# Kernel tuning notes

Measured on AMD Instinct MI355X. Metric: run time of the kernel, lower is better.

Reference implementation:

```python
import jax, jax.numpy as jnp
import numpy as np

B, S, D, H = 2, 2048, 1024, 16
HD = D // H  # head_dim = 64


def setup_inputs() -> dict:
    key = jax.random.key(0)
    ks = jax.random.split(key, 6)
    scale_h = 1.0 / np.sqrt(HD)
    scale_d = 1.0 / np.sqrt(D)
    return {
        "x": jax.random.normal(ks[0], (B, S, D), dtype=jnp.float32),
        # per-head projection weights (CausalAttention Linear(head_dim, head_dim, bias=False)), stacked over heads
        "Wq": jax.random.normal(ks[1], (H, HD, HD), dtype=jnp.float32) * scale_h,
        "Wk": jax.random.normal(ks[2], (H, HD, HD), dtype=jnp.float32) * scale_h,
        "Wv": jax.random.normal(ks[3], (H, HD, HD), dtype=jnp.float32) * scale_h,
        # final nn.Linear(dim, dim): y = x @ Wo + bo (Wo stored already transposed vs torch)
        "Wo": jax.random.normal(ks[4], (D, D), dtype=jnp.float32) * scale_d,
        "bo": jax.random.normal(ks[5], (D,), dtype=jnp.float32) * 0.01,
    }


def reference(x, Wq, Wk, Wv, Wo, bo):
    b, s, d = x.shape
    h, hd, _ = Wq.shape
    # head h sees contiguous channel slice x[:, :, h*hd:(h+1)*hd]
    xh = x.reshape(b, s, h, hd)                                  # [B,S,H,HD]
    q = jnp.einsum("bshd,hde->bhse", xh, Wq)                     # [B,H,S,HD]
    k = jnp.einsum("bshd,hde->bhse", xh, Wk)
    v = jnp.einsum("bshd,hde->bhse", xh, Wv)
    scores = jnp.einsum("bhse,bhte->bhst", q, k) * (hd ** -0.5)  # [B,H,S,S]
    causal = jnp.tril(jnp.ones((s, s), dtype=bool))
    scores = jnp.where(causal, scores, jnp.finfo(scores.dtype).min)
    attn = jax.nn.softmax(scores, axis=-1)
    out = jnp.einsum("bhst,bhtd->bshd", attn, v)                 # [B,S,H,HD]
    # torch.stack(out_list, dim=-1) -> [B,S,HD,H]; reshape -> interleaved channels
    out = jnp.swapaxes(out, -1, -2).reshape(b, s, d)
    return out @ Wo + bo
```

## Files before the change

kernel.cpp:

```cpp
#include <hip/hip_runtime.h>

typedef __attribute__((ext_vector_type(8))) _Float16 half8;
typedef __attribute__((ext_vector_type(2))) __fp16 fp16x2;
typedef __attribute__((ext_vector_type(4))) float f32x4;
typedef __attribute__((ext_vector_type(16))) float f32x16;

constexpr int Bc = 2, Sc = 2048, Dc = 1024, Hc = 16, HDc = 64;

#define PKU(a, b) __builtin_bit_cast(unsigned, __builtin_amdgcn_cvt_pkrtz((a), (b)))

#define PACK_STORE(vA0, vA1, vA2, vA3, vB0, vB1, vB2, vB3, ptr) {        \
  unsigned W0 = PKU(vA0, vA1), W1 = PKU(vA2, vA3);                       \
  unsigned X0 = PKU(vB0, vB1), X1 = PKU(vB2, vB3);                       \
  unsigned s0_ = (unsigned)__shfl_xor((int)(hi ? W0 : X0), 32);          \
  unsigned s1_ = (unsigned)__shfl_xor((int)(hi ? W1 : X1), 32);          \
  union { unsigned u[4]; half8 h8; } P_;                                 \
  P_.u[0] = hi ? s0_ : W0; P_.u[1] = hi ? s1_ : W1;                      \
  P_.u[2] = hi ? X0 : s0_; P_.u[3] = hi ? X1 : s1_;                      \
  *(half8*)(ptr) = P_.h8; }

__global__ __launch_bounds__(256) void prep_w(const float* __restrict__ Wq,
                                              const float* __restrict__ Wk,
                                              const float* __restrict__ Wv,
                                              _Float16* __restrict__ WT) {
  const int m = blockIdx.x >> 4;
  const int h = blockIdx.x & 15;
  const float* src = (m == 0 ? Wq : (m == 1 ? Wk : Wv)) + (size_t)h * 4096;
  const float scale = (m == 0) ? 0.125f * 1.44269504088896f : 1.0f;
  __shared__ float T[64][65];
  const int tid = threadIdx.x;
#pragma unroll
  for (int i = 0; i < 4; ++i) {
    int r = (tid >> 4) + 16 * i, c4 = (tid & 15) * 4;
    *(float4*)&T[r][c4] = *(const float4*)(src + r * 64 + c4);
  }
  __syncthreads();
  _Float16* dst = WT + ((size_t)m * 16 + h) * 4096;
#pragma unroll
  for (int i = 0; i < 4; ++i) {
    int e = (tid >> 4) + 16 * i, d4 = (tid & 15) * 4;
    union { _Float16 hh[4]; unsigned long long u; } pk;
#pragma unroll
    for (int j = 0; j < 4; ++j) pk.hh[j] = (_Float16)(T[d4 + j][e] * scale);
    *(unsigned long long*)(dst + (size_t)e * 64 + d4) = pk.u;
  }
}

__global__ __launch_bounds__(256) void prep_wo(const float* __restrict__ Wo,
                                               _Float16* __restrict__ WoT) {
  __shared__ float T[64][68];
  const int hh = blockIdx.x;
  const int n0 = blockIdx.y * 64;
  const int tid = threadIdx.x;
#pragma unroll
  for (int i = 0; i < 4; ++i) {
    int g = tid + i * 256;
    int e = g >> 4, c4 = (g & 15) * 4;
    *(float4*)&T[e][c4] = *(const float4*)(Wo + (size_t)(e * 16 + hh) * Dc + n0 + c4);
  }
  __syncthreads();
#pragma unroll
  for (int i = 0; i < 4; ++i) {
    int g = tid + i * 256;
    int c = g >> 4, e4 = (g & 15) * 4;
    union { _Float16 h[4]; unsigned long long u; } pk;
    pk.h[0] = (_Float16)T[e4 + 0][c];
    pk.h[1] = (_Float16)T[e4 + 1][c];
    pk.h[2] = (_Float16)T[e4 + 2][c];
    pk.h[3] = (_Float16)T[e4 + 3][c];
    *(unsigned long long*)(WoT + (size_t)(n0 + c) * Dc + hh * 64 + e4) = pk.u;
  }
}

__global__ __launch_bounds__(256) void qkv_proj(
    const float* __restrict__ x, const _Float16* __restrict__ WT,
    _Float16* __restrict__ Qp, _Float16* __restrict__ Kp,
    _Float16* __restrict__ Vp) {
  const int h = blockIdx.x & 15;
  const int st = (blockIdx.x >> 4) & 15;
  const int b = blockIdx.x >> 8;
  const int s0 = st * 128;
  const int tid = threadIdx.x;
  const int l = tid & 63, w = tid >> 6;
  const int lq = l & 31, hi = l >> 5;

  half8 xa[4];
  const float* xrow = x + ((size_t)(b * Sc + s0 + 32 * w + lq)) * Dc + h * 64 + hi * 8;
#pragma unroll
  for (int c = 0; c < 4; ++c) {
    float4 u0 = *(const float4*)(xrow + c * 16);
    float4 u1 = *(const float4*)(xrow + c * 16 + 4);
    union { fp16x2 h2[4]; half8 h8; } pk;
    pk.h2[0] = __builtin_amdgcn_cvt_pkrtz(u0.x, u0.y);
    pk.h2[1] = __builtin_amdgcn_cvt_pkrtz(u0.z, u0.w);
    pk.h2[2] = __builtin_amdgcn_cvt_pkrtz(u1.x, u1.y);
    pk.h2[3] = __builtin_amdgcn_cvt_pkrtz(u1.z, u1.w);
    xa[c] = pk.h8;
  }

  const _Float16* WTq = WT + (size_t)h * 4096;
  const _Float16* WTk = WT + (size_t)(16 + h) * 4096;
  const _Float16* WTv = WT + (size_t)(32 + h) * 4096;
  f32x16 Qt[2] = {}, Kt[2] = {}, Vd[2] = {};
#pragma unroll
  for (int et = 0; et < 2; ++et) {
#pragma unroll
    for (int c = 0; c < 4; ++c) {
      const int off = (32 * et + lq) * 64 + c * 16 + hi * 8;
      half8 wqf = *(const half8*)(WTq + off);
      half8 wkf = *(const half8*)(WTk + off);
      half8 wvf = *(const half8*)(WTv + off);
      Qt[et] = __builtin_amdgcn_mfma_f32_32x32x16_f16(wqf, xa[c], Qt[et], 0, 0, 0);
      Kt[et] = __builtin_amdgcn_mfma_f32_32x32x16_f16(wkf, xa[c], Kt[et], 0, 0, 0);
      Vd[et] = __builtin_amdgcn_mfma_f32_32x32x16_f16(xa[c], wvf, Vd[et], 0, 0, 0);
    }
  }
  const int bh = b * Hc + h;
  const int qt_ = 4 * st + w;
  const int ktile = 2 * st + (w >> 1);
  _Float16* qdst = Qp + (((size_t)(bh * 64 + qt_) * 4) << 9) + (l << 3);
  _Float16* kdst = Kp + (((size_t)((bh * 32 + ktile) * 8) + (w & 1) * 4) << 9) + (l << 3);
  _Float16* vdst = Vp + (((size_t)(bh * 32 + ktile) * 8) << 9) + (l << 3);

  PACK_STORE(Qt[0][0], Qt[0][1], Qt[0][2], Qt[0][3], Qt[0][4], Qt[0][5], Qt[0][6], Qt[0][7], qdst + (0 << 9));
  PACK_STORE(Qt[0][8], Qt[0][9], Qt[0][10], Qt[0][11], Qt[0][12], Qt[0][13], Qt[0][14], Qt[0][15], qdst + (1 << 9));
  PACK_STORE(Qt[1][0], Qt[1][1], Qt[1][2], Qt[1][3], Qt[1][4], Qt[1][5], Qt[1][6], Qt[1][7], qdst + (2 << 9));
  PACK_STORE(Qt[1][8], Qt[1][9], Qt[1][10], Qt[1][11], Qt[1][12], Qt[1][13], Qt[1][14], Qt[1][15], qdst + (3 << 9));

  PACK_STORE(Kt[0][0], Kt[0][1], Kt[0][2], Kt[0][3], Kt[0][4], Kt[0][5], Kt[0][6], Kt[0][7], kdst + (0 << 9));
  PACK_STORE(Kt[0][8], Kt[0][9], Kt[0][10], Kt[0][11], Kt[0][12], Kt[0][13], Kt[0][14], Kt[0][15], kdst + (1 << 9));
  PACK_STORE(Kt[1][0], Kt[1][1], Kt[1][2], Kt[1][3], Kt[1][4], Kt[1][5], Kt[1][6], Kt[1][7], kdst + (2 << 9));
  PACK_STORE(Kt[1][8], Kt[1][9], Kt[1][10], Kt[1][11], Kt[1][12], Kt[1][13], Kt[1][14], Kt[1][15], kdst + (3 << 9));

#pragma unroll
  for (int et = 0; et < 2; ++et) {
    PACK_STORE(Vd[et][0], Vd[et][1], Vd[et][2], Vd[et][3], Vd[et][4], Vd[et][5], Vd[et][6], Vd[et][7],
               vdst + ((size_t)(et * 4 + ((2 * w + 0) & 3)) << 9));
    PACK_STORE(Vd[et][8], Vd[et][9], Vd[et][10], Vd[et][11], Vd[et][12], Vd[et][13], Vd[et][14], Vd[et][15],
               vdst + ((size_t)(et * 4 + ((2 * w + 1) & 3)) << 9));
  }
}

#define DOB(t, q0v) (((t) * 64 + 32) <= (q0v) + 31)

#define LOADQ(qtv) {                                                          \
  const _Float16* qb_ = Qp + (((size_t)(bh * 64 + (qtv)) * 4) << 9) + (l << 3); \
  _Pragma("unroll") for (int c = 0; c < 4; ++c)                               \
    qf[c] = *(const half8*)(qb_ + (c << 9)); }

#define STEP(t, q0v) {                                                        \
  const int k0 = (t) * 64;                                                    \
  const bool doB = DOB(t, q0v);                                               \
  const int q_g = (q0v) + lq;                                                 \
  const _Float16* kp8 = Kp + (((kvb + (t)) * 8) << 9) + (l << 3);             \
  const _Float16* vp8 = Vp + (((kvb + (t)) * 8) << 9) + (l << 3);             \
  f32x16 SA = {}, SB = {};                                                    \
  {                                                                           \
    half8 ka[4], kb[4];                                                       \
    _Pragma("unroll") for (int c = 0; c < 4; ++c)                             \
      ka[c] = *(const half8*)(kp8 + (c << 9));                                \
    if (doB) {                                                                \
      _Pragma("unroll") for (int c = 0; c < 4; ++c)                           \
        kb[c] = *(const half8*)(kp8 + ((4 + c) << 9));                        \
    }                                                                         \
    __builtin_amdgcn_s_setprio(1);                                            \
    _Pragma("unroll") for (int c = 0; c < 4; ++c)                             \
      SA = __builtin_amdgcn_mfma_f32_32x32x16_f16(ka[c], qf[c], SA, 0, 0, 0); \
    if (doB) {                                                                \
      _Pragma("unroll") for (int c = 0; c < 4; ++c)                           \
        SB = __builtin_amdgcn_mfma_f32_32x32x16_f16(kb[c], qf[c], SB, 0, 0, 0); \
    }                                                                         \
    __builtin_amdgcn_s_setprio(0);                                            \
  }                                                                           \
  if (k0 + 63 > (q0v)) {                                                      \
    _Pragma("unroll") for (int r = 0; r < 16; ++r) {                          \
      const int kk = k0 + (r & 3) + 8 * (r >> 2) + 4 * hi;                    \
      if (kk > q_g) SA[r] = -1e30f;                                           \
      if (doB && kk + 32 > q_g) SB[r] = -1e30f;                               \
    }                                                                         \
  }                                                                           \
  float mx = -1e30f;                                                          \
  _Pragma("unroll") for (int r = 0; r < 16; ++r) mx = fmaxf(mx, SA[r]);       \
  if (doB) {                                                                  \
    _Pragma("unroll") for (int r = 0; r < 16; ++r) mx = fmaxf(mx, SB[r]);     \
  }                                                                           \
  mx = fmaxf(mx, __shfl_xor(mx, 32));                                         \
  if (!__all(mx <= m_run + 4.0f)) {                                           \
    const float mnew = fmaxf(m_run, mx);                                      \
    const float corr = __builtin_amdgcn_exp2f(m_run - mnew);                  \
    l_run *= corr;                                                            \
    _Pragma("unroll") for (int r = 0; r < 16; ++r) { OA[r] *= corr; OB[r] *= corr; } \
    m_run = mnew;                                                             \
  }                                                                           \
  float ls = 0.f;                                                             \
  _Pragma("unroll") for (int ch = 0; ch < 4; ++ch) {                          \
    if (ch < (doB ? 4 : 2)) {                                                 \
      half8 va = *(const half8*)(vp8 + (ch << 9));                            \
      half8 vb = *(const half8*)(vp8 + ((4 + ch) << 9));                      \
      float p0, p1, p2, p3, p4, p5, p6, p7;                                   \
      if (ch < 2) {                                                           \
        const int base = ch * 8;                                              \
        p0 = __builtin_amdgcn_exp2f(SA[base + 0] - m_run);                    \
        p1 = __builtin_amdgcn_exp2f(SA[base + 1] - m_run);                    \
        p2 = __builtin_amdgcn_exp2f(SA[base + 2] - m_run);                    \
        p3 = __builtin_amdgcn_exp2f(SA[base + 3] - m_run);                    \
        p4 = __builtin_amdgcn_exp2f(SA[base + 4] - m_run);                    \
        p5 = __builtin_amdgcn_exp2f(SA[base + 5] - m_run);                    \
        p6 = __builtin_amdgcn_exp2f(SA[base + 6] - m_run);                    \
        p7 = __builtin_amdgcn_exp2f(SA[base + 7] - m_run);                    \
      } else {                                                                \
        const int base = (ch - 2) * 8;                                        \
        p0 = __builtin_amdgcn_exp2f(SB[base + 0] - m_run);                    \
        p1 = __builtin_amdgcn_exp2f(SB[base + 1] - m_run);                    \
        p2 = __builtin_amdgcn_exp2f(SB[base + 2] - m_run);                    \
        p3 = __builtin_amdgcn_exp2f(SB[base + 3] - m_run);                    \
        p4 = __builtin_amdgcn_exp2f(SB[base + 4] - m_run);                    \
        p5 = __builtin_amdgcn_exp2f(SB[base + 5] - m_run);                    \
        p6 = __builtin_amdgcn_exp2f(SB[base + 6] - m_run);                    \
        p7 = __builtin_amdgcn_exp2f(SB[base + 7] - m_run);                    \
      }                                                                       \
      ls += ((p0 + p1) + (p2 + p3)) + ((p4 + p5) + (p6 + p7));                \
      unsigned W0 = PKU(p0, p1), W1 = PKU(p2, p3);                            \
      unsigned W2 = PKU(p4, p5), W3 = PKU(p6, p7);                            \
      unsigned sw0 = (unsigned)__shfl_xor((int)(hi ? W0 : W2), 32);           \
      unsigned sw1 = (unsigned)__shfl_xor((int)(hi ? W1 : W3), 32);           \
      union { unsigned u[4]; half8 h; } pa;                                   \
      pa.u[0] = hi ? sw0 : W0;                                                \
      pa.u[1] = hi ? sw1 : W1;                                                \
      pa.u[2] = hi ? W2 : sw0;                                                \
      pa.u[3] = hi ? W3 : sw1;                                                \
      __builtin_amdgcn_s_setprio(1);                                          \
      OA = __builtin_amdgcn_mfma_f32_32x32x16_f16(va, pa.h, OA, 0, 0, 0);     \
      OB = __builtin_amdgcn_mfma_f32_32x32x16_f16(vb, pa.h, OB, 0, 0, 0);     \
      __builtin_amdgcn_s_setprio(0);                                          \
    }                                                                         \
  }                                                                           \
  ls += __shfl_xor(ls, 32);                                                   \
  l_run += ls; }

#define RUN_RANGE(t0, t1, q0v) {                                              \
  for (int t = (t0); t < (t1); ++t) { STEP(t, q0v); } }

#define PUBLISH(slot) {                                                       \
  _Pragma("unroll") for (int r = 0; r < 16; ++r) {                            \
    Osh[slot][l][r] = OA[r]; Osh[slot][l][16 + r] = OB[r];                    \
  }                                                                           \
  mls[slot][0][l] = m_run; mls[slot][1][l] = l_run; }

#define RESET() {                                                             \
  _Pragma("unroll") for (int r = 0; r < 16; ++r) { OA[r] = 0.f; OB[r] = 0.f; } \
  m_run = -1e30f; l_run = 0.f; }

#define MERGE(slot) {                                                         \
  const float ms = mls[slot][0][l], lsv = mls[slot][1][l];                    \
  const float mm = fmaxf(m_run, ms);                                          \
  const float c0 = __builtin_amdgcn_exp2f(m_run - mm);                        \
  const float c1 = __builtin_amdgcn_exp2f(ms - mm);                           \
  _Pragma("unroll") for (int r = 0; r < 16; ++r) {                            \
    OA[r] = OA[r] * c0 + Osh[slot][l][r] * c1;                                \
    OB[r] = OB[r] * c0 + Osh[slot][l][16 + r] * c1;                           \
  }                                                                           \
  l_run = l_run * c0 + lsv * c1; m_run = mm; }

#define STORE_OUT(q0v) {                                                      \
  const float inv = 1.f / l_run;                                              \
  _Float16* op = attC + ((size_t)b * Sc + (q0v) + lq) * Dc + h * 64;          \
  _Pragma("unroll") for (int g = 0; g < 4; ++g) {                             \
    union { _Float16 hh[4]; unsigned long long u; } pA, pB;                   \
    _Pragma("unroll") for (int jj = 0; jj < 4; ++jj) {                        \
      pA.hh[jj] = (_Float16)(OA[4 * g + jj] * inv);                           \
      pB.hh[jj] = (_Float16)(OB[4 * g + jj] * inv);                           \
    }                                                                         \
    *(unsigned long long*)(op + 8 * g + 4 * hi) = pA.u;                       \
    *(unsigned long long*)(op + 32 + 8 * g + 4 * hi) = pB.u;                  \
  } }

__global__ __launch_bounds__(256, 3) void flash_attn(
    const _Float16* __restrict__ Qp, const _Float16* __restrict__ Kp,
    const _Float16* __restrict__ Vp, _Float16* __restrict__ attC) {
  const int i = blockIdx.x;
  const int bh = (i & 7) * 4 + ((i >> 3) & 3);
  const int p = i >> 5;
  const int qlong = 63 - p, qshort = p;
  const int NTL = qlong / 2 + 1;
  const int NTS = qshort / 2 + 1;
  const int q0L = qlong * 32, q0S = qshort * 32;
  const int b = bh >> 4, h = bh & 15;
  const int tid = threadIdx.x;
  const int wv = tid >> 6, l = tid & 63;
  const int lq = l & 31, hi = l >> 5;
  const size_t kvb = (size_t)bh * 32;

  __shared__ float Osh[3][64][33];
  __shared__ float mls[3][2][64];

  half8 qf[4];
  f32x16 OA = {}, OB = {};
  float m_run = -1e30f, l_run = 0.f;

  if (wv == 0) {
    LOADQ(qlong);
    RUN_RANGE(0, 8, q0L);
  } else if (wv == 1) {
    LOADQ(qlong);
    RUN_RANGE(8, 16, q0L);
    PUBLISH(0);
  } else if (wv == 2) {
    LOADQ(qlong);
    const int e2 = NTL < 24 ? NTL : 24;
    RUN_RANGE(16, e2, q0L);
    PUBLISH(1);
    RESET();
    if (24 - NTL > 0) {
      LOADQ(qshort);
      RUN_RANGE(0, 24 - NTL, q0S);
    }
  } else {
    if (NTL > 24) {
      LOADQ(qlong);
      RUN_RANGE(24, NTL, q0L);
      PUBLISH(2);
      RESET();
      LOADQ(qshort);
      RUN_RANGE(0, NTS, q0S);
      STORE_OUT(q0S);
    } else {
      LOADQ(qshort);
      RUN_RANGE(24 - NTL, NTS, q0S);
      PUBLISH(2);
    }
  }
  __syncthreads();
  if (wv == 0) {
    MERGE(0);
    MERGE(1);
    if (NTL > 24) { MERGE(2); }
    STORE_OUT(q0L);
  } else if (wv == 2 && NTL <= 24) {
    MERGE(2);
    STORE_OUT(q0S);
  }
}

__global__ __launch_bounds__(256) void out_proj(
    const _Float16* __restrict__ attC, const _Float16* __restrict__ WoT,
    const float* __restrict__ bo, float* __restrict__ out) {
  const int m0 = blockIdx.x * 64, n0 = blockIdx.y * 64;
  __shared__ __align__(16) _Float16 Alds[64][40];
  __shared__ __align__(16) _Float16 Blds[64][40];
  const int tid = threadIdx.x;
  const int l = tid & 63, w = tid >> 6;
  const int lr = l & 15, lg = l >> 4;
  f32x4 acc[4] = {};
  for (int kt = 0; kt < 32; ++kt) {
    const int k0 = kt * 32;
    {
      const int r = tid >> 2, c8 = (tid & 3) * 8;
      *(half8*)&Alds[r][c8] = *(const half8*)(attC + (size_t)(m0 + r) * Dc + k0 + c8);
      *(half8*)&Blds[r][c8] = *(const half8*)(WoT + (size_t)(n0 + r) * Dc + k0 + c8);
    }
    __syncthreads();
    half8 bf = *(const half8*)&Blds[w * 16 + lr][lg * 8];
#pragma unroll
    for (int i2 = 0; i2 < 4; ++i2) {
      half8 af = *(const half8*)&Alds[i2 * 16 + lr][lg * 8];
      acc[i2] = __builtin_amdgcn_mfma_f32_16x16x32_f16(af, bf, acc[i2], 0, 0, 0);
    }
    __syncthreads();
  }
  const int n = n0 + w * 16 + lr;
  const float bias = bo[n];
#pragma unroll
  for (int i2 = 0; i2 < 4; ++i2)
#pragma unroll
    for (int r = 0; r < 4; ++r) {
      const int m = m0 + i2 * 16 + lg * 4 + r;
      out[(size_t)m * Dc + n] = acc[i2][r] + bias;
    }
}

extern "C" void kernel_launch(void* const* d_in, const int* in_sizes, int n_in,
                              void* d_out, int out_size, void* d_ws, size_t ws_size,
                              hipStream_t stream) {
  const float* x  = (const float*)d_in[0];
  const float* Wq = (const float*)d_in[1];
  const float* Wk = (const float*)d_in[2];
  const float* Wv = (const float*)d_in[3];
  const float* Wo = (const float*)d_in[4];
  const float* bo = (const float*)d_in[5];
  float* out = (float*)d_out;
  char* ws = (char*)d_ws;
  _Float16* Qp   = (_Float16*)(ws);
  _Float16* Kp   = (_Float16*)(ws + (size_t)(8  << 20));
  _Float16* Vp   = (_Float16*)(ws + (size_t)(16 << 20));
  _Float16* WoT  = (_Float16*)(ws + (size_t)(24 << 20));
  _Float16* WT   = (_Float16*)(ws + (size_t)(26 << 20));
  _Float16* attC = (_Float16*)(ws + (size_t)(26 << 20));

  prep_w<<<dim3(48), dim3(256), 0, stream>>>(Wq, Wk, Wv, WT);
  prep_wo<<<dim3(16, 16), dim3(256), 0, stream>>>(Wo, WoT);
  qkv_proj<<<dim3(512), dim3(256), 0, stream>>>(x, WT, Qp, Kp, Vp);
  flash_attn<<<dim3(1024), dim3(256), 0, stream>>>(Qp, Kp, Vp, attC);
  out_proj<<<dim3(64, 16), dim3(256), 0, stream>>>(attC, WoT, bo, out);
}
```

Before: 86.91 us.

## Stage x via swizzled LDS, hoist V loads, widen out_proj N tile

Three independent changes. qkv_proj now loads x coalesced into a swizzled shared-memory tile before building its MFMA fragments, replacing strided per-lane global reads. flash_attn issues all V fragment loads early, before masking and softmax, so their latency overlaps that work; this costs more registers. out_proj doubles its N tile to 128 so each A fragment feeds two MFMAs, halving the grid and the A traffic per output.

```diff
diff --git a/kernel.cpp b/kernel.cpp
--- a/kernel.cpp
+++ b/kernel.cpp
@@ -6,6 +6,10 @@
 typedef __attribute__((ext_vector_type(16))) float f32x16;
 
 constexpr int Bc = 2, Sc = 2048, Dc = 1024, Hc = 16, HDc = 64;
+
+__device__ __forceinline__ int swz(int row, int colh) {
+  return row * 64 + (colh ^ ((row & 7) * 8));
+}
 
 #define PKU(a, b) __builtin_bit_cast(unsigned, __builtin_amdgcn_cvt_pkrtz((a), (b)))
 
@@ -80,23 +84,29 @@
   const int st = (blockIdx.x >> 4) & 15;
   const int b = blockIdx.x >> 8;
   const int s0 = st * 128;
+  __shared__ __align__(16) _Float16 xs[128 * 64];
   const int tid = threadIdx.x;
-  const int l = tid & 63, w = tid >> 6;
-  const int lq = l & 31, hi = l >> 5;
-
-  half8 xa[4];
-  const float* xrow = x + ((size_t)(b * Sc + s0 + 32 * w + lq)) * Dc + h * 64 + hi * 8;
-#pragma unroll
-  for (int c = 0; c < 4; ++c) {
-    float4 u0 = *(const float4*)(xrow + c * 16);
-    float4 u1 = *(const float4*)(xrow + c * 16 + 4);
+#pragma unroll
+  for (int i = 0; i < 4; ++i) {
+    int r = (tid >> 3) + 32 * i;
+    int c8 = (tid & 7) * 8;
+    const float* xp = x + ((size_t)(b * Sc + s0 + r)) * Dc + h * 64 + c8;
+    float4 u0 = *(const float4*)xp;
+    float4 u1 = *(const float4*)(xp + 4);
     union { fp16x2 h2[4]; half8 h8; } pk;
     pk.h2[0] = __builtin_amdgcn_cvt_pkrtz(u0.x, u0.y);
     pk.h2[1] = __builtin_amdgcn_cvt_pkrtz(u0.z, u0.w);
     pk.h2[2] = __builtin_amdgcn_cvt_pkrtz(u1.x, u1.y);
     pk.h2[3] = __builtin_amdgcn_cvt_pkrtz(u1.z, u1.w);
-    xa[c] = pk.h8;
-  }
+    *(half8*)&xs[swz(r, c8)] = pk.h8;
+  }
+  __syncthreads();
+  const int l = tid & 63, w = tid >> 6;
+  const int lq = l & 31, hi = l >> 5;
+  half8 xa[4];
+#pragma unroll
+  for (int c = 0; c < 4; ++c)
+    xa[c] = *(const half8*)&xs[swz(32 * w + lq, c * 16 + hi * 8)];
 
   const _Float16* WTq = WT + (size_t)h * 4096;
   const _Float16* WTk = WT + (size_t)(16 + h) * 4096;
@@ -148,7 +158,7 @@
   _Pragma("unroll") for (int c = 0; c < 4; ++c)                               \
     qf[c] = *(const half8*)(qb_ + (c << 9)); }
 
-#define STEP(t, q0v) {                                                        \
+#define STEP(t, q0v) {                                                       \
   const int k0 = (t) * 64;                                                    \
   const bool doB = DOB(t, q0v);                                               \
   const int q_g = (q0v) + lq;                                                 \
@@ -172,6 +182,18 @@
     }                                                                         \
     __builtin_amdgcn_s_setprio(0);                                            \
   }                                                                           \
+       \
+  half8 va[4], vb[4];                                                         \
+  va[0] = *(const half8*)(vp8 + (0 << 9));                                    \
+  va[1] = *(const half8*)(vp8 + (1 << 9));                                    \
+  vb[0] = *(const half8*)(vp8 + (4 << 9));                                    \
+  vb[1] = *(const half8*)(vp8 + (5 << 9));                                    \
+  if (doB) {                                                                  \
+    va[2] = *(const half8*)(vp8 + (2 << 9));                                  \
+    va[3] = *(const half8*)(vp8 + (3 << 9));                                  \
+    vb[2] = *(const half8*)(vp8 + (6 << 9));                                  \
+    vb[3] = *(const half8*)(vp8 + (7 << 9));                                  \
+  }                                                                           \
   if (k0 + 63 > (q0v)) {                                                      \
     _Pragma("unroll") for (int r = 0; r < 16; ++r) {                          \
       const int kk = k0 + (r & 3) + 8 * (r >> 2) + 4 * hi;                    \
@@ -195,8 +217,6 @@
   float ls = 0.f;                                                             \
   _Pragma("unroll") for (int ch = 0; ch < 4; ++ch) {                          \
     if (ch < (doB ? 4 : 2)) {                                                 \
-      half8 va = *(const half8*)(vp8 + (ch << 9));                            \
-      half8 vb = *(const half8*)(vp8 + ((4 + ch) << 9));                      \
       float p0, p1, p2, p3, p4, p5, p6, p7;                                   \
       if (ch < 2) {                                                           \
         const int base = ch * 8;                                              \
@@ -230,8 +250,8 @@
       pa.u[2] = hi ? W2 : sw0;                                                \
       pa.u[3] = hi ? W3 : sw1;                                                \
       __builtin_amdgcn_s_setprio(1);                                          \
-      OA = __builtin_amdgcn_mfma_f32_32x32x16_f16(va, pa.h, OA, 0, 0, 0);     \
-      OB = __builtin_amdgcn_mfma_f32_32x32x16_f16(vb, pa.h, OB, 0, 0, 0);     \
+      OA = __builtin_amdgcn_mfma_f32_32x32x16_f16(va[ch], pa.h, OA, 0, 0, 0); \
+      OB = __builtin_amdgcn_mfma_f32_32x32x16_f16(vb[ch], pa.h, OB, 0, 0, 0); \
       __builtin_amdgcn_s_setprio(0);                                          \
     }                                                                         \
   }                                                                           \
@@ -345,37 +365,49 @@
 __global__ __launch_bounds__(256) void out_proj(
     const _Float16* __restrict__ attC, const _Float16* __restrict__ WoT,
     const float* __restrict__ bo, float* __restrict__ out) {
-  const int m0 = blockIdx.x * 64, n0 = blockIdx.y * 64;
+  const int m0 = blockIdx.x * 64, n0 = blockIdx.y * 128;
   __shared__ __align__(16) _Float16 Alds[64][40];
-  __shared__ __align__(16) _Float16 Blds[64][40];
+  __shared__ __align__(16) _Float16 Blds[128][40];
   const int tid = threadIdx.x;
   const int l = tid & 63, w = tid >> 6;
   const int lr = l & 15, lg = l >> 4;
-  f32x4 acc[4] = {};
+  f32x4 acc[4][2] = {};
   for (int kt = 0; kt < 32; ++kt) {
     const int k0 = kt * 32;
     {
       const int r = tid >> 2, c8 = (tid & 3) * 8;
       *(half8*)&Alds[r][c8] = *(const half8*)(attC + (size_t)(m0 + r) * Dc + k0 + c8);
-      *(half8*)&Blds[r][c8] = *(const half8*)(WoT + (size_t)(n0 + r) * Dc + k0 + c8);
+#pragma unroll
+      for (int ii = 0; ii < 2; ++ii) {
+        const int g = tid + ii * 256;
+        const int rb = g >> 2, cb = (g & 3) * 8;
+        *(half8*)&Blds[rb][cb] = *(const half8*)(WoT + (size_t)(n0 + rb) * Dc + k0 + cb);
+      }
     }
     __syncthreads();
-    half8 bf = *(const half8*)&Blds[w * 16 + lr][lg * 8];
-#pragma unroll
-    for (int i2 = 0; i2 < 4; ++i2) {
-      half8 af = *(const half8*)&Alds[i2 * 16 + lr][lg * 8];
-      acc[i2] = __builtin_amdgcn_mfma_f32_16x16x32_f16(af, bf, acc[i2], 0, 0, 0);
-    }
+    half8 af[4], bf[2];
+#pragma unroll
+    for (int i2 = 0; i2 < 4; ++i2) af[i2] = *(const half8*)&Alds[i2 * 16 + lr][lg * 8];
+#pragma unroll
+    for (int j = 0; j < 2; ++j) bf[j] = *(const half8*)&Blds[w * 32 + j * 16 + lr][lg * 8];
+#pragma unroll
+    for (int i2 = 0; i2 < 4; ++i2)
+#pragma unroll
+      for (int j = 0; j < 2; ++j)
+        acc[i2][j] = __builtin_amdgcn_mfma_f32_16x16x32_f16(af[i2], bf[j], acc[i2][j], 0, 0, 0);
     __syncthreads();
   }
-  const int n = n0 + w * 16 + lr;
-  const float bias = bo[n];
 #pragma unroll
   for (int i2 = 0; i2 < 4; ++i2)
 #pragma unroll
-    for (int r = 0; r < 4; ++r) {
-      const int m = m0 + i2 * 16 + lg * 4 + r;
-      out[(size_t)m * Dc + n] = acc[i2][r] + bias;
+    for (int j = 0; j < 2; ++j) {
+      const int n = n0 + w * 32 + j * 16 + lr;
+      const float bias = bo[n];
+#pragma unroll
+      for (int r = 0; r < 4; ++r) {
+        const int m = m0 + i2 * 16 + lg * 4 + r;
+        out[(size_t)m * Dc + n] = acc[i2][j][r] + bias;
+      }
     }
 }
 
@@ -401,5 +433,5 @@
   prep_wo<<<dim3(16, 16), dim3(256), 0, stream>>>(Wo, WoT);
   qkv_proj<<<dim3(512), dim3(256), 0, stream>>>(x, WT, Qp, Kp, Vp);
   flash_attn<<<dim3(1024), dim3(256), 0, stream>>>(Qp, Kp, Vp, attC);
-  out_proj<<<dim3(64, 16), dim3(256), 0, stream>>>(attC, WoT, bo, out);
-}
+  out_proj<<<dim3(64, 8), dim3(256), 0, stream>>>(attC, WoT, bo, out);
+}
```

Result: no change. 85.31 us (-1.8%).
